# Performance work log

Measured on AMD Instinct MI355X. Metric: run time of the kernel, lower is better.

## Reference

```python
import jax, jax.numpy as jnp
import numpy as np

B = 16      # graphs
NPG = 1024  # nodes per graph (equal-sized, contiguous)
N = B * NPG
K = 12      # knn neighbors
DM = 128    # d_model
DH = 256    # d_hidden = 2*d_model
L = 3       # num_layers
DI = 2 * DM + 4  # msg mlp input dim


def _mlp2(x, W1, b1, W2, b2):
    return jax.nn.silu(x @ W1 + b1) @ W2 + b2


def setup_inputs() -> dict:
    key = jax.random.key(0)
    ks = list(jax.random.split(key, 16))
    def nrm(k, shape, fan):
        return jax.random.normal(k, shape, jnp.float32) / np.float32(np.sqrt(fan))
    return dict(
        x=jax.random.normal(ks[0], (N, 3), jnp.float32),
        batch=(jnp.arange(N) // NPG).astype(jnp.int32),
        in_W1=nrm(ks[1], (3, DM), 3), in_b1=jnp.zeros((DM,), jnp.float32),
        in_W2=nrm(ks[2], (DM, DM), DM), in_b2=jnp.zeros((DM,), jnp.float32),
        msg_W1=nrm(ks[3], (L, DI, DH), DI), msg_b1=jnp.zeros((L, DH), jnp.float32),
        msg_W2=nrm(ks[4], (L, DH, DM), DH), msg_b2=jnp.zeros((L, DM), jnp.float32),
        upd_W1=nrm(ks[5], (L, 2 * DM, DH), 2 * DM), upd_b1=jnp.zeros((L, DH), jnp.float32),
        upd_W2=nrm(ks[6], (L, DH, DM), DH), upd_b2=jnp.zeros((L, DM), jnp.float32),
        norm_w=jnp.ones((L, DM), jnp.float32), norm_b=jnp.zeros((L, DM), jnp.float32),
        norm_ms=jnp.ones((L, DM), jnp.float32),
        gate_W1=nrm(ks[7], (DM, DM), DM), gate_b1=jnp.zeros((DM,), jnp.float32),
        gate_W2=nrm(ks[8], (DM, 1), DM), gate_b2=jnp.zeros((1,), jnp.float32),
        head_W1=nrm(ks[9], (DM, DM), DM), head_b1=jnp.zeros((DM,), jnp.float32),
        head_W2=nrm(ks[10], (DM, 1), DM), head_b2=jnp.zeros((1,), jnp.float32),
    )


def _knn_edges(pos):
    # pos: [N,2]; graphs are contiguous blocks of NPG nodes -> blocked knn
    p3 = pos.reshape(B, NPG, 2)
    d2 = jnp.sum((p3[:, :, None, :] - p3[:, None, :, :]) ** 2, axis=-1)  # [B,n,n]
    d2 = jnp.where(jnp.eye(NPG, dtype=bool)[None], jnp.inf, d2)          # no self loops
    idx = jax.lax.top_k(-d2, K)[1]  # [B,n,K] nearest neighbors (sources)
    offs = (jnp.arange(B) * NPG)[:, None, None]
    src = (idx + offs).reshape(-1)
    dst = jnp.broadcast_to(jnp.arange(N).reshape(B, NPG, 1), (B, NPG, K)).reshape(-1)
    return src, dst


def _graph_norm(h, batch, cnt, w, b, ms):
    # PyG GraphNorm: out = w * (h - ms*mean) / sqrt(var + eps) + b, per-graph stats
    mean = jax.ops.segment_sum(h, batch, B) / cnt
    out = h - mean[batch] * ms
    var = jax.ops.segment_sum(out ** 2, batch, B) / cnt
    return w * out / jnp.sqrt(var + 1e-5)[batch] + b


def _forward(x, batch, in_W1, in_b1, in_W2, in_b2, msg_W1, msg_b1, msg_W2, msg_b2,
             upd_W1, upd_b1, upd_W2, upd_b2, norm_w, norm_b, norm_ms,
             gate_W1, gate_b1, gate_W2, gate_b2, head_W1, head_b1, head_W2, head_b2):
    pos = x[:, 1:3]
    src, dst = _knn_edges(pos)
    # edge_attr = [dx, dy, dist, ds]
    dp = pos[src] - pos[dst]
    dist = jnp.sqrt(jnp.sum(dp ** 2, axis=-1, keepdims=True) + 1e-12)
    ds = x[src, 0:1] - x[dst, 0:1]
    ea = jnp.concatenate([dp, dist, ds], axis=-1)  # [E,4]

    h = _mlp2(x, in_W1, in_b1, in_W2, in_b2)       # [N,DM]
    cnt = jax.ops.segment_sum(jnp.ones((N,), h.dtype), batch, B)[:, None]

    for i in range(L):
        m_in = jnp.concatenate([h[dst], h[src], ea], axis=-1)       # [E,2*DM+4]
        m = _mlp2(m_in, msg_W1[i], msg_b1[i], msg_W2[i], msg_b2[i])  # [E,DM]
        agg = jax.ops.segment_sum(m, dst, N)                         # scatter_add
        dh = _mlp2(jnp.concatenate([h, agg], axis=-1),
                   upd_W1[i], upd_b1[i], upd_W2[i], upd_b2[i])
        h = h + dh  # dropout is identity at inference
        h = _graph_norm(h, batch, cnt, norm_w[i], norm_b[i], norm_ms[i])

    # gated attention pool: segment softmax over gate logits
    gl = (jnp.tanh(h @ gate_W1 + gate_b1) @ gate_W2 + gate_b2)[:, 0]  # [N]
    gmax = jax.ops.segment_max(gl, batch, B)
    e = jnp.exp(gl - gmax[batch])
    a = e / jax.ops.segment_sum(e, batch, B)[batch]
    pooled = jax.ops.segment_sum(h * a[:, None], batch, B)            # [B,DM]

    return _mlp2(pooled, head_W1, head_b1, head_W2, head_b2)[:, 0]    # [B]


def reference(x, batch, in_W1, in_b1, in_W2, in_b2, msg_W1, msg_b1, msg_W2, msg_b2,
              upd_W1, upd_b1, upd_W2, upd_b2, norm_w, norm_b, norm_ms,
              gate_W1, gate_b1, gate_W2, gate_b2, head_W1, head_b1, head_W2, head_b2):
    return _forward(x, batch, in_W1, in_b1, in_W2, in_b2, msg_W1, msg_b1, msg_W2, msg_b2,
                    upd_W1, upd_b1, upd_W2, upd_b2, norm_w, norm_b, norm_ms,
                    gate_W1, gate_b1, gate_W2, gate_b2, head_W1, head_b1, head_W2, head_b2)
```

## Files before the change

kernel.cpp:

```cpp
#include <hip/hip_runtime.h>
#include <math.h>

#define NPTS 16384
#define BGR 16
#define NPGR 1024
#define KNN 12
#define DM 128
#define DH 256
#define NL 3
#define EDG (NPTS*KNN)

typedef unsigned short u16;
typedef unsigned int u32;
typedef __attribute__((ext_vector_type(8))) short short8;
typedef __attribute__((ext_vector_type(4))) float floatx4;

__device__ __forceinline__ float silu_f(float x) {
    return x / (1.0f + __expf(-x));
}
__device__ __forceinline__ u16 f2bf(float f) {
    union { float f; u32 u; } v; v.f = f;
    u32 r = v.u + 0x7fffu + ((v.u >> 16) & 1u);
    return (u16)(r >> 16);
}
__device__ __forceinline__ float bf2f(u16 b) {
    union { u32 u; float f; } v; v.u = ((u32)b) << 16;
    return v.f;
}

#define KPPB 32
__global__ __launch_bounds__(256) void knn_kernel(const float* __restrict__ x,
                                                  int* __restrict__ srcb,
                                                  float* __restrict__ ea) {
#pragma clang fp contract(off)
    __shared__ float px[NPGR], py[NPGR], s0[NPGR];
    __shared__ float sdf[256 * 13];
    __shared__ int   sif[256 * 13];
    __shared__ int   sel[KPPB][KNN];
    int t = threadIdx.x;
    int g   = blockIdx.x / (NPGR / KPPB);
    int blk = blockIdx.x % (NPGR / KPPB);
    int base = g * NPGR;
    for (int j = t; j < NPGR; j += 256) {
        const float* xp = x + (size_t)(base + j) * 3;
        s0[j] = xp[0]; px[j] = xp[1]; py[j] = xp[2];
    }
    __syncthreads();
    int r  = t & 7;
    int pt = t >> 3;
    int il = blk * KPPB + pt;
    float xi = px[il], yi = py[il];
    float nd[KNN]; int ni[KNN];
#pragma unroll
    for (int k = 0; k < KNN; ++k) { nd[k] = 3.4e38f; ni[k] = 0x7fffffff; }
    int j0 = r * 128;
    for (int jj = 0; jj < 128; ++jj) {
        int j = j0 + jj;
        if (j == il) continue;
        float dx = px[j] - xi;
        float dy = py[j] - yi;
        float dx2 = dx * dx;
        float dy2 = dy * dy;
        float d2 = dx2 + dy2;
        if (d2 < nd[KNN-1]) {
            float cd = d2; int ci = j;
#pragma unroll
            for (int k = 0; k < KNN; ++k) {
                bool sw = cd < nd[k];
                float tdv = sw ? nd[k] : cd;
                nd[k] = sw ? cd : nd[k];
                cd = tdv;
                int tiv = sw ? ni[k] : ci;
                ni[k] = sw ? ci : ni[k];
                ci = tiv;
            }
        }
    }
#pragma unroll
    for (int k = 0; k < KNN; ++k) { sdf[t * 13 + k] = nd[k]; sif[t * 13 + k] = ni[k]; }
    __syncthreads();
    if (r == 0) {
        int head[8] = {0,0,0,0,0,0,0,0};
#pragma unroll
        for (int k = 0; k < KNN; ++k) {
            float bd = 3.4e38f; int bi = 0x7fffffff; int bq = 0;
#pragma unroll
            for (int q = 0; q < 8; ++q) {
                int hq = head[q];
                float d = (hq < KNN) ? sdf[(pt * 8 + q) * 13 + hq] : 3.4e38f;
                int  ix = (hq < KNN) ? sif[(pt * 8 + q) * 13 + hq] : 0x7fffffff;
                if (d < bd || (d == bd && ix < bi)) { bd = d; bi = ix; bq = q; }
            }
            head[bq]++;
            sel[pt][k] = bi;
        }
    }
    __syncthreads();
    float x0i = s0[il];
    for (int k = r; k < KNN; k += 8) {
        int j = sel[pt][k];
        size_t e = (size_t)(base + il) * KNN + k;
        srcb[e] = base + j;
        float dpx = px[j] - xi, dpy = py[j] - yi;
        float a = dpx * dpx;
        float b = dpy * dpy;
        float dist = sqrtf(a + b + 1e-12f);
        float dsv = s0[j] - x0i;
        *(float4*)(ea + e * 4) = make_float4(dpx, dpy, dist, dsv);
    }
}

__global__ __launch_bounds__(128) void in_mlp_kernel(const float* __restrict__ x,
    const float* __restrict__ W1, const float* __restrict__ b1,
    const float* __restrict__ W2, const float* __restrict__ b2,
    float* __restrict__ h) {
    __shared__ float hid[8][DM];
    __shared__ float xl[8][3];
    int t = threadIdx.x;
    int nb = blockIdx.x * 8;
    if (t < 24) xl[t / 3][t % 3] = x[(size_t)nb * 3 + t];
    __syncthreads();
    float w0 = W1[t], w1 = W1[DM + t], w2 = W1[2 * DM + t], bb = b1[t];
#pragma unroll
    for (int gi = 0; gi < 8; ++gi) {
        float v = xl[gi][0] * w0 + xl[gi][1] * w1 + xl[gi][2] * w2 + bb;
        hid[gi][t] = silu_f(v);
    }
    __syncthreads();
    float acc[8];
    float b2v = b2[t];
#pragma unroll
    for (int gi = 0; gi < 8; ++gi) acc[gi] = b2v;
    for (int k = 0; k < DM; ++k) {
        float w = W2[k * DM + t];
#pragma unroll
        for (int gi = 0; gi < 8; ++gi) acc[gi] += hid[gi][k] * w;
    }
#pragma unroll
    for (int gi = 0; gi < 8; ++gi) h[(size_t)(nb + gi) * DM + t] = acc[gi];
}

#define MBM 128
#define MBN 128
#define MBK 32
#define MLDA 40

__global__ __launch_bounds__(256) void mgemm_kernel(
    const float* __restrict__ A0, int k0, int lda0,
    const float* __restrict__ A1, int lda1,
    const u16* __restrict__ Wh, const u16* __restrict__ Wl, int K,
    const float* __restrict__ bias,
    const float* __restrict__ resid, int ldres,
    float* __restrict__ out, int ldout,
    int act)
{
    __shared__ __align__(16) u16 Ash[MBM * MLDA];
    __shared__ __align__(16) u16 Asl[MBM * MLDA];
    __shared__ __align__(16) u16 Bsh[MBN * MLDA];
    __shared__ __align__(16) u16 Bsl[MBN * MLDA];
    int t = threadIdx.x;
    int row0 = blockIdx.x * MBM, col0 = blockIdx.y * MBN;
    int lane = t & 63, w = t >> 6;
    int wm = (w >> 1) * 64, wn = (w & 1) * 64;
    int quad = lane >> 4, r15 = lane & 15;
    int srow = t >> 1, scol = (t & 1) * 16;

    floatx4 acc[4][4];
#pragma unroll
    for (int m = 0; m < 4; ++m)
#pragma unroll
        for (int n = 0; n < 4; ++n) acc[m][n] = (floatx4){0.f, 0.f, 0.f, 0.f};

    for (int kt = 0; kt < K; kt += MBK) {
        const float* Ap = (kt < k0)
            ? (A0 + (size_t)(row0 + srow) * lda0 + kt + scol)
            : (A1 + (size_t)(row0 + srow) * lda1 + (kt - k0) + scol);
        float4 a0 = ((const float4*)Ap)[0];
        float4 a1 = ((const float4*)Ap)[1];
        float4 a2 = ((const float4*)Ap)[2];
        float4 a3 = ((const float4*)Ap)[3];
        const u16* Bph = Wh + (size_t)(col0 + srow) * K + kt + scol;
        const u16* Bpl = Wl + (size_t)(col0 + srow) * K + kt + scol;
        uint4 bh0 = ((const uint4*)Bph)[0];
        uint4 bh1 = ((const uint4*)Bph)[1];
        uint4 bl0 = ((const uint4*)Bpl)[0];
        uint4 bl1 = ((const uint4*)Bpl)[1];
        __syncthreads();
        float av[16] = {a0.x,a0.y,a0.z,a0.w, a1.x,a1.y,a1.z,a1.w,
                        a2.x,a2.y,a2.z,a2.w, a3.x,a3.y,a3.z,a3.w};
        u32 uh[8], ul[8];
#pragma unroll
        for (int i = 0; i < 8; ++i) {
            u16 h0 = f2bf(av[2*i]);
            u16 h1 = f2bf(av[2*i+1]);
            u16 l0 = f2bf(av[2*i]   - bf2f(h0));
            u16 l1 = f2bf(av[2*i+1] - bf2f(h1));
            uh[i] = (u32)h0 | ((u32)h1 << 16);
            ul[i] = (u32)l0 | ((u32)l1 << 16);
        }
        uint4* adh = (uint4*)(Ash + srow * MLDA + scol);
        uint4* adl = (uint4*)(Asl + srow * MLDA + scol);
        adh[0] = make_uint4(uh[0],uh[1],uh[2],uh[3]);
        adh[1] = make_uint4(uh[4],uh[5],uh[6],uh[7]);
        adl[0] = make_uint4(ul[0],ul[1],ul[2],ul[3]);
        adl[1] = make_uint4(ul[4],ul[5],ul[6],ul[7]);
        uint4* bdh = (uint4*)(Bsh + srow * MLDA + scol);
        uint4* bdl = (uint4*)(Bsl + srow * MLDA + scol);
        bdh[0] = bh0; bdh[1] = bh1;
        bdl[0] = bl0; bdl[1] = bl1;
        __syncthreads();
        short8 ah[4], alo[4], bhf[4], blf[4];
#pragma unroll
        for (int m = 0; m < 4; ++m) {
            ah[m]  = *(const short8*)(Ash + (wm + m*16 + r15) * MLDA + quad*8);
            alo[m] = *(const short8*)(Asl + (wm + m*16 + r15) * MLDA + quad*8);
        }
#pragma unroll
        for (int n = 0; n < 4; ++n) {
            bhf[n] = *(const short8*)(Bsh + (wn + n*16 + r15) * MLDA + quad*8);
            blf[n] = *(const short8*)(Bsl + (wn + n*16 + r15) * MLDA + quad*8);
        }
#pragma unroll
        for (int m = 0; m < 4; ++m)
#pragma unroll
            for (int n = 0; n < 4; ++n) {
                acc[m][n] = __builtin_amdgcn_mfma_f32_16x16x32_bf16(ah[m],  bhf[n], acc[m][n], 0, 0, 0);
                acc[m][n] = __builtin_amdgcn_mfma_f32_16x16x32_bf16(ah[m],  blf[n], acc[m][n], 0, 0, 0);
                acc[m][n] = __builtin_amdgcn_mfma_f32_16x16x32_bf16(alo[m], bhf[n], acc[m][n], 0, 0, 0);
            }
    }
#pragma unroll
    for (int n = 0; n < 4; ++n) {
        int col = col0 + wn + n*16 + r15;
        float bv = bias ? bias[col] : 0.f;
#pragma unroll
        for (int m = 0; m < 4; ++m) {
#pragma unroll
            for (int reg = 0; reg < 4; ++reg) {
                int row = row0 + wm + m*16 + quad*4 + reg;
                float v = acc[m][n][reg] + bv;
                if (act == 1) v = silu_f(v);
                else if (act == 2) v = tanhf(v);
                if (resid) v += resid[(size_t)row * ldres + col];
                out[(size_t)row * ldout + col] = v;
            }
        }
    }
}

__global__ __launch_bounds__(256) void edge_agg_kernel(
    const float* __restrict__ C, const float* __restrict__ S,
    const int* __restrict__ srcb, const float* __restrict__ ea,
    const float* __restrict__ W1ea,
    float* __restrict__ HS)
{
    int i = blockIdx.x, t = threadIdx.x;
    __shared__ int ss[KNN];
    __shared__ float sea[KNN * 4];
    if (t < KNN) ss[t] = srcb[(size_t)i * KNN + t];
    if (t < KNN * 4) sea[t] = ea[(size_t)i * KNN * 4 + t];
    __syncthreads();
    float base = C[(size_t)i * DH + t];
    float wa = W1ea[t], wb = W1ea[DH + t], wc = W1ea[2 * DH + t], wd = W1ea[3 * DH + t];
    float hs = 0.f;
#pragma unroll
    for (int e = 0; e < KNN; ++e) {
        float v = base + S[(size_t)ss[e] * DH + t]
                + sea[e * 4 + 0] * wa + sea[e * 4 + 1] * wb
                + sea[e * 4 + 2] * wc + sea[e * 4 + 3] * wd;
        hs += silu_f(v);
    }
    HS[(size_t)i * DH + t] = hs;
}

__global__ __launch_bounds__(256) void norm_part_kernel(const float* __restrict__ hn,
                                                        float* __restrict__ psum)
{
    int g = blockIdx.x, blk = blockIdx.y;
    int t = threadIdx.x, d = t & 127, half = t >> 7;
    size_t base = ((size_t)g * NPGR + (size_t)blk * 128 + half * 64) * DM;
    float s = 0.f, s2 = 0.f;
    for (int n = 0; n < 64; ++n) {
        float v = hn[base + (size_t)n * DM + d];
        s += v; s2 += v * v;
    }
    __shared__ float ps[2][DM], ps2[2][DM];
    ps[half][d] = s; ps2[half][d] = s2;
    __syncthreads();
    if (t < DM) {
        psum[(((size_t)g * 8 + blk) * 2 + 0) * DM + d] = ps[0][d] + ps[1][d];
        psum[(((size_t)g * 8 + blk) * 2 + 1) * DM + d] = ps2[0][d] + ps2[1][d];
    }
}

__global__ __launch_bounds__(256) void norm_apply_kernel(const float* __restrict__ hn,
    float* __restrict__ h, const float* __restrict__ psum,
    const float* __restrict__ w, const float* __restrict__ b, const float* __restrict__ ms)
{
    int g = blockIdx.x, blk = blockIdx.y, t = threadIdx.x;
    __shared__ float mmv[DM], rst[DM], wv[DM], bv[DM];
    if (t < DM) {
        float sum = 0.f, sq = 0.f;
        for (int q = 0; q < 8; ++q) {
            sum += psum[(((size_t)g * 8 + q) * 2 + 0) * DM + t];
            sq  += psum[(((size_t)g * 8 + q) * 2 + 1) * DM + t];
        }
        float mean = sum * (1.0f / NPGR);
        float mm = mean * ms[t];
        float var = sq * (1.0f / NPGR) - 2.f * mm * mean + mm * mm;
        mmv[t] = mm;
        rst[t] = 1.0f / sqrtf(var + 1e-5f);
        wv[t] = w[t]; bv[t] = b[t];
    }
    __syncthreads();
    size_t base = ((size_t)g * NPGR + (size_t)blk * 128) * DM;
    for (int i = t; i < 128 * DM; i += 256) {
        int dd = i & 127;
        float v = hn[base + i];
        h[base + i] = wv[dd] * (v - mmv[dd]) * rst[dd] + bv[dd];
    }
}

__global__ __launch_bounds__(256) void gate_dot_kernel(const float* __restrict__ Gh,
    const float* __restrict__ gW2, const float* __restrict__ gb2,
    float* __restrict__ gl)
{
    int t = threadIdx.x, lane = t & 63, w = t >> 6;
    int node = blockIdx.x * 4 + w;
    const float* gp = Gh + (size_t)node * DM;
    float v = gp[lane] * gW2[lane] + gp[lane + 64] * gW2[lane + 64];
    for (int off = 32; off > 0; off >>= 1) v += __shfl_down(v, off, 64);
    if (lane == 0) gl[node] = v + gb2[0];
}

__global__ __launch_bounds__(256) void pool_stats_kernel(const float* __restrict__ gl,
                                                         float* __restrict__ gstat)
{
    int g = blockIdx.x, t = threadIdx.x, lane = t & 63, w = t >> 6;
    __shared__ float red[4];
    const float* gp = gl + (size_t)g * NPGR;
    float mx = -3.4e38f;
    for (int n = t; n < NPGR; n += 256) mx = fmaxf(mx, gp[n]);
    for (int off = 32; off > 0; off >>= 1) mx = fmaxf(mx, __shfl_down(mx, off, 64));
    if (lane == 0) red[w] = mx;
    __syncthreads();
    float gmax = fmaxf(fmaxf(red[0], red[1]), fmaxf(red[2], red[3]));
    __syncthreads();
    float se = 0.f;
    for (int n = t; n < NPGR; n += 256) se += __expf(gp[n] - gmax);
    for (int off = 32; off > 0; off >>= 1) se += __shfl_down(se, off, 64);
    if (lane == 0) red[w] = se;
    __syncthreads();
    if (t == 0) { gstat[g * 2] = gmax; gstat[g * 2 + 1] = red[0] + red[1] + red[2] + red[3]; }
}

__global__ __launch_bounds__(256) void pool_part_kernel(const float* __restrict__ h,
    const float* __restrict__ gl, const float* __restrict__ gstat,
    float* __restrict__ ppool)
{
    int g = blockIdx.x, blk = blockIdx.y;
    int t = threadIdx.x, d = t & 127, half = t >> 7;
    float gmax = gstat[g * 2];
    size_t nbase = (size_t)g * NPGR + (size_t)blk * 128 + half * 64;
    float p = 0.f;
    for (int n = 0; n < 64; ++n)
        p += __expf(gl[nbase + n] - gmax) * h[(nbase + n) * DM + d];
    __shared__ float ps[2][DM];
    ps[half][d] = p;
    __syncthreads();
    if (t < DM) ppool[((size_t)g * 8 + blk) * DM + d] = ps[0][d] + ps[1][d];
}

__global__ __launch_bounds__(128) void pool_head_kernel(const float* __restrict__ ppool,
    const float* __restrict__ gstat,
    const float* __restrict__ hW1, const float* __restrict__ hb1,
    const float* __restrict__ hW2, const float* __restrict__ hb2,
    float* __restrict__ outp)
{
    int g = blockIdx.x, t = threadIdx.x;
    __shared__ float pl[DM];
    __shared__ float red[2];
    float ssum = gstat[g * 2 + 1];
    float p = 0.f;
    for (int q = 0; q < 8; ++q) p += ppool[((size_t)g * 8 + q) * DM + t];
    pl[t] = p / ssum;
    __syncthreads();
    float a = hb1[t];
    for (int k = 0; k < DM; ++k) a += pl[k] * hW1[k * DM + t];
    a = silu_f(a);
    float vv = a * hW2[t];
    int lane = t & 63, w = t >> 6;
    for (int off = 32; off > 0; off >>= 1) vv += __shfl_down(vv, off, 64);
    if (lane == 0) red[w] = vv;
    __syncthreads();
    if (t == 0) outp[g] = red[0] + red[1] + hb2[0];
}

__global__ __launch_bounds__(256) void precompute_kernel(
    const float* __restrict__ msgW2, const float* __restrict__ msgb2,
    const float* __restrict__ updW1, const float* __restrict__ updb1,
    float* __restrict__ W2U, float* __restrict__ bias2)
{
    int bid = blockIdx.x; int t = threadIdx.x;
    if (bid < NL * DH) {
        int l = bid / DH, k = bid % DH;
        const float* w2row = msgW2 + (size_t)l * DH * DM + (size_t)k * DM;
        const float* u1 = updW1 + (size_t)l * 2 * DM * DH;
        float acc = 0.f;
        for (int j = 0; j < DM; ++j) acc += w2row[j] * u1[(size_t)(DM + j) * DH + t];
        W2U[(size_t)l * DH * DH + (size_t)k * DH + t] = acc;
    } else {
        int l = bid - NL * DH;
        const float* u1 = updW1 + (size_t)l * 2 * DM * DH;
        const float* b2 = msgb2 + (size_t)l * DM;
        float acc = updb1[(size_t)l * DH + t];
        for (int j = 0; j < DM; ++j) acc += 12.0f * b2[j] * u1[(size_t)(DM + j) * DH + t];
        bias2[(size_t)l * DH + t] = acc;
    }
}

struct WJob { const float* src; u16* dh; u16* dl; int K, N, ldd, off; };
struct WJobs { WJob j[16]; };
__global__ __launch_bounds__(256) void wprep_kernel(WJobs jobs) {
    WJob jb = jobs.j[blockIdx.y];
    int n = blockIdx.x;
    if (n >= jb.N) return;
    for (int k = threadIdx.x; k < jb.K; k += 256) {
        float v = jb.src[(size_t)k * jb.N + n];
        u16 hi = f2bf(v);
        u16 lo = f2bf(v - bf2f(hi));
        jb.dh[(size_t)n * jb.ldd + jb.off + k] = hi;
        jb.dl[(size_t)n * jb.ldd + jb.off + k] = lo;
    }
}

extern "C" void kernel_launch(void* const* d_in, const int* in_sizes, int n_in,
                              void* d_out, int out_size, void* d_ws, size_t ws_size,
                              hipStream_t stream) {
    const float* x     = (const float*)d_in[0];
    const float* inW1  = (const float*)d_in[2];
    const float* inb1  = (const float*)d_in[3];
    const float* inW2  = (const float*)d_in[4];
    const float* inb2  = (const float*)d_in[5];
    const float* msgW1 = (const float*)d_in[6];
    const float* msgb1 = (const float*)d_in[7];
    const float* msgW2 = (const float*)d_in[8];
    const float* msgb2 = (const float*)d_in[9];
    const float* updW1 = (const float*)d_in[10];
    const float* updb1 = (const float*)d_in[11];
    const float* updW2 = (const float*)d_in[12];
    const float* updb2 = (const float*)d_in[13];
    const float* nw    = (const float*)d_in[14];
    const float* nb    = (const float*)d_in[15];
    const float* nms   = (const float*)d_in[16];
    const float* gW1   = (const float*)d_in[17];
    const float* gb1   = (const float*)d_in[18];
    const float* gW2   = (const float*)d_in[19];
    const float* gb2   = (const float*)d_in[20];
    const float* hW1   = (const float*)d_in[21];
    const float* hb1   = (const float*)d_in[22];
    const float* hW2   = (const float*)d_in[23];
    const float* hb2   = (const float*)d_in[24];
    float* outp = (float*)d_out;

    float* ws    = (float*)d_ws;
    float* h     = ws;
    float* Cb    = h + (size_t)NPTS * DM;
    float* Sb    = Cb + (size_t)NPTS * DH;
    float* HSb   = Sb + (size_t)NPTS * DH;
    float* W2U   = HSb + (size_t)NPTS * DH;
    float* bias2 = W2U + (size_t)NL * DH * DH;
    float* glb   = bias2 + NL * DH;
    int*   srcb  = (int*)(glb + NPTS);
    float* eab   = (float*)(srcb + EDG);
    float* psum  = eab + (size_t)EDG * 4;
    float* gstat = psum + 16 * 8 * 2 * DM;
    float* ppool = gstat + 32;
    u16* wsp = (u16*)(ppool + 16 * 8 * DM);
    u16* WCh = wsp;                 u16* WCl = WCh + (size_t)NL * DH * DM;
    u16* WSh = WCl + (size_t)NL * DH * DM;  u16* WSl = WSh + (size_t)NL * DH * DM;
    u16* WTh = WSl + (size_t)NL * DH * DM;  u16* WTl = WTh + (size_t)NL * DH * 384;
    u16* WUh = WTl + (size_t)NL * DH * 384; u16* WUl = WUh + (size_t)NL * DM * DH;
    u16* WGh = WUl + (size_t)NL * DM * DH;  u16* WGl = WGh + (size_t)DM * DM;

    hipLaunchKernelGGL(precompute_kernel, dim3(NL * DH + NL), dim3(DH), 0, stream,
                       msgW2, msgb2, updW1, updb1, W2U, bias2);

    WJobs jobs;
    int ji = 0;
    for (int l = 0; l < NL; ++l) {
        jobs.j[ji++] = WJob{ msgW1 + (size_t)l * 260 * DH,             WCh + (size_t)l * DH * DM, WCl + (size_t)l * DH * DM, 128, 256, 128, 0 };
        jobs.j[ji++] = WJob{ msgW1 + (size_t)l * 260 * DH + 128 * DH,  WSh + (size_t)l * DH * DM, WSl + (size_t)l * DH * DM, 128, 256, 128, 0 };
        jobs.j[ji++] = WJob{ updW1 + (size_t)l * 256 * DH,             WTh + (size_t)l * DH * 384, WTl + (size_t)l * DH * 384, 128, 256, 384, 0 };
        jobs.j[ji++] = WJob{ W2U   + (size_t)l * DH * DH,              WTh + (size_t)l * DH * 384, WTl + (size_t)l * DH * 384, 256, 256, 384, 128 };
        jobs.j[ji++] = WJob{ updW2 + (size_t)l * DH * DM,              WUh + (size_t)l * DM * DH, WUl + (size_t)l * DM * DH, 256, 128, 256, 0 };
    }
    jobs.j[ji++] = WJob{ gW1, WGh, WGl, 128, 128, 128, 0 };
    hipLaunchKernelGGL(wprep_kernel, dim3(256, 16), dim3(256), 0, stream, jobs);

    hipLaunchKernelGGL(knn_kernel, dim3(NPTS / KPPB), dim3(256), 0, stream, x, srcb, eab);
    hipLaunchKernelGGL(in_mlp_kernel, dim3(NPTS / 8), dim3(128), 0, stream,
                       x, inW1, inb1, inW2, inb2, h);

    for (int l = 0; l < NL; ++l) {
        const float* W1l = msgW1 + (size_t)l * 260 * DH;
        hipLaunchKernelGGL(mgemm_kernel, dim3(NPTS / MBM, DH / MBN), dim3(256), 0, stream,
            h, DM, DM, (const float*)nullptr, 0,
            WCh + (size_t)l * DH * DM, WCl + (size_t)l * DH * DM, DM,
            msgb1 + (size_t)l * DH, (const float*)nullptr, 0, Cb, DH, 0);
        hipLaunchKernelGGL(mgemm_kernel, dim3(NPTS / MBM, DH / MBN), dim3(256), 0, stream,
            h, DM, DM, (const float*)nullptr, 0,
            WSh + (size_t)l * DH * DM, WSl + (size_t)l * DH * DM, DM,
            (const float*)nullptr, (const float*)nullptr, 0, Sb, DH, 0);
        hipLaunchKernelGGL(edge_agg_kernel, dim3(NPTS), dim3(DH), 0, stream,
            Cb, Sb, srcb, eab, W1l + (size_t)2 * DM * DH, HSb);
        hipLaunchKernelGGL(mgemm_kernel, dim3(NPTS / MBM, DH / MBN), dim3(256), 0, stream,
            h, DM, DM, HSb, DH,
            WTh + (size_t)l * DH * 384, WTl + (size_t)l * DH * 384, 384,
            bias2 + (size_t)l * DH, (const float*)nullptr, 0, Cb, DH, 1);
        hipLaunchKernelGGL(mgemm_kernel, dim3(NPTS / MBM, DM / MBN), dim3(256), 0, stream,
            Cb, DH, DH, (const float*)nullptr, 0,
            WUh + (size_t)l * DM * DH, WUl + (size_t)l * DM * DH, DH,
            updb2 + (size_t)l * DM, h, DM, Sb, DM, 0);
        hipLaunchKernelGGL(norm_part_kernel, dim3(BGR, 8), dim3(256), 0, stream, Sb, psum);
        hipLaunchKernelGGL(norm_apply_kernel, dim3(BGR, 8), dim3(256), 0, stream,
            Sb, h, psum, nw + (size_t)l * DM, nb + (size_t)l * DM, nms + (size_t)l * DM);
    }

    hipLaunchKernelGGL(mgemm_kernel, dim3(NPTS / MBM, DM / MBN), dim3(256), 0, stream,
        h, DM, DM, (const float*)nullptr, 0,
        WGh, WGl, DM, gb1, (const float*)nullptr, 0, Cb, DM, 2);
    hipLaunchKernelGGL(gate_dot_kernel, dim3(NPTS / 4), dim3(256), 0, stream,
        Cb, gW2, gb2, glb);

    hipLaunchKernelGGL(pool_stats_kernel, dim3(BGR), dim3(256), 0, stream, glb, gstat);
    hipLaunchKernelGGL(pool_part_kernel, dim3(BGR, 8), dim3(256), 0, stream, h, glb, gstat, ppool);
    hipLaunchKernelGGL(pool_head_kernel, dim3(BGR), dim3(128), 0, stream,
        ppool, gstat, hW1, hb1, hW2, hb2, outp);
}
```

Baseline: 627.1 us.

## Merge C/S projection GEMMs, halve GEMM M-tile, and split KNN scan wider

Fuses the two per-layer projection GEMMs on h into one GEMM with a concatenated 512-column weight and interleaved CS output, with bias applied only to the first 256 columns. The mgemm M-tile is halved to 64 rows to double the block count for better CU occupancy. The KNN kernel now handles 16 points per block with 16 scanning threads each, which shortens each thread's serial insertion loop but doubles the merge width. Buffers are reshuffled so the update output goes to HSb. The CS layout also gives strided reads in edge_agg.

```diff
diff --git a/kernel.cpp b/kernel.cpp
--- a/kernel.cpp
+++ b/kernel.cpp
@@ -28,14 +28,15 @@
     return v.f;
 }
 
-#define KPPB 32
+#define KPPB 16
+#define PSTR 209
 __global__ __launch_bounds__(256) void knn_kernel(const float* __restrict__ x,
                                                   int* __restrict__ srcb,
                                                   float* __restrict__ ea) {
 #pragma clang fp contract(off)
     __shared__ float px[NPGR], py[NPGR], s0[NPGR];
-    __shared__ float sdf[256 * 13];
-    __shared__ int   sif[256 * 13];
+    __shared__ float sdf[KPPB * PSTR];
+    __shared__ int   sif[KPPB * PSTR];
     __shared__ int   sel[KPPB][KNN];
     int t = threadIdx.x;
     int g   = blockIdx.x / (NPGR / KPPB);
@@ -46,15 +47,15 @@
         s0[j] = xp[0]; px[j] = xp[1]; py[j] = xp[2];
     }
     __syncthreads();
-    int r  = t & 7;
-    int pt = t >> 3;
+    int r  = t & 15;
+    int pt = t >> 4;
     int il = blk * KPPB + pt;
     float xi = px[il], yi = py[il];
     float nd[KNN]; int ni[KNN];
 #pragma unroll
     for (int k = 0; k < KNN; ++k) { nd[k] = 3.4e38f; ni[k] = 0x7fffffff; }
-    int j0 = r * 128;
-    for (int jj = 0; jj < 128; ++jj) {
+    int j0 = r * 64;
+    for (int jj = 0; jj < 64; ++jj) {
         int j = j0 + jj;
         if (j == il) continue;
         float dx = px[j] - xi;
@@ -77,18 +78,23 @@
         }
     }
 #pragma unroll
-    for (int k = 0; k < KNN; ++k) { sdf[t * 13 + k] = nd[k]; sif[t * 13 + k] = ni[k]; }
+    for (int k = 0; k < KNN; ++k) {
+        sdf[pt * PSTR + r * 13 + k] = nd[k];
+        sif[pt * PSTR + r * 13 + k] = ni[k];
+    }
     __syncthreads();
     if (r == 0) {
-        int head[8] = {0,0,0,0,0,0,0,0};
+        int head[16];
+#pragma unroll
+        for (int q = 0; q < 16; ++q) head[q] = 0;
 #pragma unroll
         for (int k = 0; k < KNN; ++k) {
             float bd = 3.4e38f; int bi = 0x7fffffff; int bq = 0;
 #pragma unroll
-            for (int q = 0; q < 8; ++q) {
+            for (int q = 0; q < 16; ++q) {
                 int hq = head[q];
-                float d = (hq < KNN) ? sdf[(pt * 8 + q) * 13 + hq] : 3.4e38f;
-                int  ix = (hq < KNN) ? sif[(pt * 8 + q) * 13 + hq] : 0x7fffffff;
+                float d = (hq < KNN) ? sdf[pt * PSTR + q * 13 + hq] : 3.4e38f;
+                int  ix = (hq < KNN) ? sif[pt * PSTR + q * 13 + hq] : 0x7fffffff;
                 if (d < bd || (d == bd && ix < bi)) { bd = d; bi = ix; bq = q; }
             }
             head[bq]++;
@@ -96,11 +102,12 @@
         }
     }
     __syncthreads();
-    float x0i = s0[il];
-    for (int k = r; k < KNN; k += 8) {
+    if (r < KNN) {
+        int k = r;
         int j = sel[pt][k];
         size_t e = (size_t)(base + il) * KNN + k;
         srcb[e] = base + j;
+        float x0i = s0[il];
         float dpx = px[j] - xi, dpy = py[j] - yi;
         float a = dpx * dpx;
         float b = dpy * dpy;
@@ -140,7 +147,7 @@
     for (int gi = 0; gi < 8; ++gi) h[(size_t)(nb + gi) * DM + t] = acc[gi];
 }
 
-#define MBM 128
+#define MBM 64
 #define MBN 128
 #define MBK 32
 #define MLDA 40
@@ -149,7 +156,7 @@
     const float* __restrict__ A0, int k0, int lda0,
     const float* __restrict__ A1, int lda1,
     const u16* __restrict__ Wh, const u16* __restrict__ Wl, int K,
-    const float* __restrict__ bias,
+    const float* __restrict__ bias, int biasN,
     const float* __restrict__ resid, int ldres,
     float* __restrict__ out, int ldout,
     int act)
@@ -161,36 +168,34 @@
     int t = threadIdx.x;
     int row0 = blockIdx.x * MBM, col0 = blockIdx.y * MBN;
     int lane = t & 63, w = t >> 6;
-    int wm = (w >> 1) * 64, wn = (w & 1) * 64;
+    int wm = (w >> 1) * 32, wn = (w & 1) * 64;
     int quad = lane >> 4, r15 = lane & 15;
-    int srow = t >> 1, scol = (t & 1) * 16;
-
-    floatx4 acc[4][4];
-#pragma unroll
-    for (int m = 0; m < 4; ++m)
+    int arow = t >> 2, acol = (t & 3) * 8;
+    int brow = t >> 1, bcol = (t & 1) * 16;
+
+    floatx4 acc[2][4];
+#pragma unroll
+    for (int m = 0; m < 2; ++m)
 #pragma unroll
         for (int n = 0; n < 4; ++n) acc[m][n] = (floatx4){0.f, 0.f, 0.f, 0.f};
 
     for (int kt = 0; kt < K; kt += MBK) {
         const float* Ap = (kt < k0)
-            ? (A0 + (size_t)(row0 + srow) * lda0 + kt + scol)
-            : (A1 + (size_t)(row0 + srow) * lda1 + (kt - k0) + scol);
+            ? (A0 + (size_t)(row0 + arow) * lda0 + kt + acol)
+            : (A1 + (size_t)(row0 + arow) * lda1 + (kt - k0) + acol);
         float4 a0 = ((const float4*)Ap)[0];
         float4 a1 = ((const float4*)Ap)[1];
-        float4 a2 = ((const float4*)Ap)[2];
-        float4 a3 = ((const float4*)Ap)[3];
-        const u16* Bph = Wh + (size_t)(col0 + srow) * K + kt + scol;
-        const u16* Bpl = Wl + (size_t)(col0 + srow) * K + kt + scol;
+        const u16* Bph = Wh + (size_t)(col0 + brow) * K + kt + bcol;
+        const u16* Bpl = Wl + (size_t)(col0 + brow) * K + kt + bcol;
         uint4 bh0 = ((const uint4*)Bph)[0];
         uint4 bh1 = ((const uint4*)Bph)[1];
         uint4 bl0 = ((const uint4*)Bpl)[0];
         uint4 bl1 = ((const uint4*)Bpl)[1];
         __syncthreads();
-        float av[16] = {a0.x,a0.y,a0.z,a0.w, a1.x,a1.y,a1.z,a1.w,
-                        a2.x,a2.y,a2.z,a2.w, a3.x,a3.y,a3.z,a3.w};
-        u32 uh[8], ul[8];
-#pragma unroll
-        for (int i = 0; i < 8; ++i) {
+        float av[8] = {a0.x,a0.y,a0.z,a0.w, a1.x,a1.y,a1.z,a1.w};
+        u32 uh[4], ul[4];
+#pragma unroll
+        for (int i = 0; i < 4; ++i) {
             u16 h0 = f2bf(av[2*i]);
             u16 h1 = f2bf(av[2*i+1]);
             u16 l0 = f2bf(av[2*i]   - bf2f(h0));
@@ -198,20 +203,16 @@
             uh[i] = (u32)h0 | ((u32)h1 << 16);
             ul[i] = (u32)l0 | ((u32)l1 << 16);
         }
-        uint4* adh = (uint4*)(Ash + srow * MLDA + scol);
-        uint4* adl = (uint4*)(Asl + srow * MLDA + scol);
-        adh[0] = make_uint4(uh[0],uh[1],uh[2],uh[3]);
-        adh[1] = make_uint4(uh[4],uh[5],uh[6],uh[7]);
-        adl[0] = make_uint4(ul[0],ul[1],ul[2],ul[3]);
-        adl[1] = make_uint4(ul[4],ul[5],ul[6],ul[7]);
-        uint4* bdh = (uint4*)(Bsh + srow * MLDA + scol);
-        uint4* bdl = (uint4*)(Bsl + srow * MLDA + scol);
+        *(uint4*)(Ash + arow * MLDA + acol) = make_uint4(uh[0],uh[1],uh[2],uh[3]);
+        *(uint4*)(Asl + arow * MLDA + acol) = make_uint4(ul[0],ul[1],ul[2],ul[3]);
+        uint4* bdh = (uint4*)(Bsh + brow * MLDA + bcol);
+        uint4* bdl = (uint4*)(Bsl + brow * MLDA + bcol);
         bdh[0] = bh0; bdh[1] = bh1;
         bdl[0] = bl0; bdl[1] = bl1;
         __syncthreads();
-        short8 ah[4], alo[4], bhf[4], blf[4];
-#pragma unroll
-        for (int m = 0; m < 4; ++m) {
+        short8 ah[2], alo[2], bhf[4], blf[4];
+#pragma unroll
+        for (int m = 0; m < 2; ++m) {
             ah[m]  = *(const short8*)(Ash + (wm + m*16 + r15) * MLDA + quad*8);
             alo[m] = *(const short8*)(Asl + (wm + m*16 + r15) * MLDA + quad*8);
         }
@@ -221,7 +222,7 @@
             blf[n] = *(const short8*)(Bsl + (wn + n*16 + r15) * MLDA + quad*8);
         }
 #pragma unroll
-        for (int m = 0; m < 4; ++m)
+        for (int m = 0; m < 2; ++m)
 #pragma unroll
             for (int n = 0; n < 4; ++n) {
                 acc[m][n] = __builtin_amdgcn_mfma_f32_16x16x32_bf16(ah[m],  bhf[n], acc[m][n], 0, 0, 0);
@@ -232,9 +233,9 @@
 #pragma unroll
     for (int n = 0; n < 4; ++n) {
         int col = col0 + wn + n*16 + r15;
-        float bv = bias ? bias[col] : 0.f;
-#pragma unroll
-        for (int m = 0; m < 4; ++m) {
+        float bv = (bias && col < biasN) ? bias[col] : 0.f;
+#pragma unroll
+        for (int m = 0; m < 2; ++m) {
 #pragma unroll
             for (int reg = 0; reg < 4; ++reg) {
                 int row = row0 + wm + m*16 + quad*4 + reg;
@@ -249,7 +250,7 @@
 }
 
 __global__ __launch_bounds__(256) void edge_agg_kernel(
-    const float* __restrict__ C, const float* __restrict__ S,
+    const float* __restrict__ CS,
     const int* __restrict__ srcb, const float* __restrict__ ea,
     const float* __restrict__ W1ea,
     float* __restrict__ HS)
@@ -260,12 +261,12 @@
     if (t < KNN) ss[t] = srcb[(size_t)i * KNN + t];
     if (t < KNN * 4) sea[t] = ea[(size_t)i * KNN * 4 + t];
     __syncthreads();
-    float base = C[(size_t)i * DH + t];
+    float base = CS[(size_t)i * 512 + t];
     float wa = W1ea[t], wb = W1ea[DH + t], wc = W1ea[2 * DH + t], wd = W1ea[3 * DH + t];
     float hs = 0.f;
 #pragma unroll
     for (int e = 0; e < KNN; ++e) {
-        float v = base + S[(size_t)ss[e] * DH + t]
+        float v = base + CS[(size_t)ss[e] * 512 + 256 + t]
                 + sea[e * 4 + 0] * wa + sea[e * 4 + 1] * wb
                 + sea[e * 4 + 2] * wc + sea[e * 4 + 3] * wd;
         hs += silu_f(v);
@@ -465,9 +466,8 @@
 
     float* ws    = (float*)d_ws;
     float* h     = ws;
-    float* Cb    = h + (size_t)NPTS * DM;
-    float* Sb    = Cb + (size_t)NPTS * DH;
-    float* HSb   = Sb + (size_t)NPTS * DH;
+    float* CSb   = h + (size_t)NPTS * DM;
+    float* HSb   = CSb + (size_t)NPTS * 512;
     float* W2U   = HSb + (size_t)NPTS * DH;
     float* bias2 = W2U + (size_t)NL * DH * DH;
     float* glb   = bias2 + NL * DH;
@@ -477,11 +477,10 @@
     float* gstat = psum + 16 * 8 * 2 * DM;
     float* ppool = gstat + 32;
     u16* wsp = (u16*)(ppool + 16 * 8 * DM);
-    u16* WCh = wsp;                 u16* WCl = WCh + (size_t)NL * DH * DM;
-    u16* WSh = WCl + (size_t)NL * DH * DM;  u16* WSl = WSh + (size_t)NL * DH * DM;
-    u16* WTh = WSl + (size_t)NL * DH * DM;  u16* WTl = WTh + (size_t)NL * DH * 384;
-    u16* WUh = WTl + (size_t)NL * DH * 384; u16* WUl = WUh + (size_t)NL * DM * DH;
-    u16* WGh = WUl + (size_t)NL * DM * DH;  u16* WGl = WGh + (size_t)DM * DM;
+    u16* WCSh = wsp;                                 u16* WCSl = WCSh + (size_t)NL * 512 * DM;
+    u16* WTh = WCSl + (size_t)NL * 512 * DM;         u16* WTl = WTh + (size_t)NL * DH * 384;
+    u16* WUh = WTl + (size_t)NL * DH * 384;          u16* WUl = WUh + (size_t)NL * DM * DH;
+    u16* WGh = WUl + (size_t)NL * DM * DH;           u16* WGl = WGh + (size_t)DM * DM;
 
     hipLaunchKernelGGL(precompute_kernel, dim3(NL * DH + NL), dim3(DH), 0, stream,
                        msgW2, msgb2, updW1, updb1, W2U, bias2);
@@ -489,11 +488,11 @@
     WJobs jobs;
     int ji = 0;
     for (int l = 0; l < NL; ++l) {
-        jobs.j[ji++] = WJob{ msgW1 + (size_t)l * 260 * DH,             WCh + (size_t)l * DH * DM, WCl + (size_t)l * DH * DM, 128, 256, 128, 0 };
-        jobs.j[ji++] = WJob{ msgW1 + (size_t)l * 260 * DH + 128 * DH,  WSh + (size_t)l * DH * DM, WSl + (size_t)l * DH * DM, 128, 256, 128, 0 };
-        jobs.j[ji++] = WJob{ updW1 + (size_t)l * 256 * DH,             WTh + (size_t)l * DH * 384, WTl + (size_t)l * DH * 384, 128, 256, 384, 0 };
-        jobs.j[ji++] = WJob{ W2U   + (size_t)l * DH * DH,              WTh + (size_t)l * DH * 384, WTl + (size_t)l * DH * 384, 256, 256, 384, 128 };
-        jobs.j[ji++] = WJob{ updW2 + (size_t)l * DH * DM,              WUh + (size_t)l * DM * DH, WUl + (size_t)l * DM * DH, 256, 128, 256, 0 };
+        jobs.j[ji++] = WJob{ msgW1 + (size_t)l * 260 * DH,            WCSh + (size_t)l * 512 * DM,            WCSl + (size_t)l * 512 * DM,            128, 256, 128, 0 };
+        jobs.j[ji++] = WJob{ msgW1 + (size_t)l * 260 * DH + 128 * DH, WCSh + (size_t)l * 512 * DM + 256 * DM, WCSl + (size_t)l * 512 * DM + 256 * DM, 128, 256, 128, 0 };
+        jobs.j[ji++] = WJob{ updW1 + (size_t)l * 256 * DH,            WTh + (size_t)l * DH * 384, WTl + (size_t)l * DH * 384, 128, 256, 384, 0 };
+        jobs.j[ji++] = WJob{ W2U   + (size_t)l * DH * DH,             WTh + (size_t)l * DH * 384, WTl + (size_t)l * DH * 384, 256, 256, 384, 128 };
+        jobs.j[ji++] = WJob{ updW2 + (size_t)l * DH * DM,             WUh + (size_t)l * DM * DH, WUl + (size_t)l * DM * DH, 256, 128, 256, 0 };
     }
     jobs.j[ji++] = WJob{ gW1, WGh, WGl, 128, 128, 128, 0 };
     hipLaunchKernelGGL(wprep_kernel, dim3(256, 16), dim3(256), 0, stream, jobs);
@@ -504,34 +503,30 @@
 
     for (int l = 0; l < NL; ++l) {
         const float* W1l = msgW1 + (size_t)l * 260 * DH;
-        hipLaunchKernelGGL(mgemm_kernel, dim3(NPTS / MBM, DH / MBN), dim3(256), 0, stream,
+        hipLaunchKernelGGL(mgemm_kernel, dim3(NPTS / MBM, 512 / MBN), dim3(256), 0, stream,
             h, DM, DM, (const float*)nullptr, 0,
-            WCh + (size_t)l * DH * DM, WCl + (size_t)l * DH * DM, DM,
-            msgb1 + (size_t)l * DH, (const float*)nullptr, 0, Cb, DH, 0);
-        hipLaunchKernelGGL(mgemm_kernel, dim3(NPTS / MBM, DH / MBN), dim3(256), 0, stream,
-            h, DM, DM, (const float*)nullptr, 0,
-            WSh + (size_t)l * DH * DM, WSl + (size_t)l * DH * DM, DM,
-            (const float*)nullptr, (const float*)nullptr, 0, Sb, DH, 0);
+            WCSh + (size_t)l * 512 * DM, WCSl + (size_t)l * 512 * DM, DM,
+            msgb1 + (size_t)l * DH, 256, (const float*)nullptr, 0, CSb, 512, 0);
         hipLaunchKernelGGL(edge_agg_kernel, dim3(NPTS), dim3(DH), 0, stream,
-            Cb, Sb, srcb, eab, W1l + (size_t)2 * DM * DH, HSb);
+            CSb, srcb, eab, W1l + (size_t)2 * DM * DH, HSb);
         hipLaunchKernelGGL(mgemm_kernel, dim3(NPTS / MBM, DH / MBN), dim3(256), 0, stream,
             h, DM, DM, HSb, DH,
             WTh + (size_t)l * DH * 384, WTl + (size_t)l * DH * 384, 384,
-            bias2 + (size_t)l * DH, (const float*)nullptr, 0, Cb, DH, 1);
+            bias2 + (size_t)l * DH, DH, (const float*)nullptr, 0, CSb, 512, 1);
         hipLaunchKernelGGL(mgemm_kernel, dim3(NPTS / MBM, DM / MBN), dim3(256), 0, stream,
-            Cb, DH, DH, (const float*)nullptr, 0,
+            CSb, 512, 512, (const float*)nullptr, 0,
             WUh + (size_t)l * DM * DH, WUl + (size_t)l * DM * DH, DH,
-            updb2 + (size_t)l * DM, h, DM, Sb, DM, 0);
-        hipLaunchKernelGGL(norm_part_kernel, dim3(BGR, 8), dim3(256), 0, stream, Sb, psum);
+            updb2 + (size_t)l * DM, DM, h, DM, HSb, DM, 0);
+        hipLaunchKernelGGL(norm_part_kernel, dim3(BGR, 8), dim3(256), 0, stream, HSb, psum);
         hipLaunchKernelGGL(norm_apply_kernel, dim3(BGR, 8), dim3(256), 0, stream,
-            Sb, h, psum, nw + (size_t)l * DM, nb + (size_t)l * DM, nms + (size_t)l * DM);
+            HSb, h, psum, nw + (size_t)l * DM, nb + (size_t)l * DM, nms + (size_t)l * DM);
     }
 
     hipLaunchKernelGGL(mgemm_kernel, dim3(NPTS / MBM, DM / MBN), dim3(256), 0, stream,
         h, DM, DM, (const float*)nullptr, 0,
-        WGh, WGl, DM, gb1, (const float*)nullptr, 0, Cb, DM, 2);
+        WGh, WGl, DM, gb1, DM, (const float*)nullptr, 0, CSb, DM, 2);
     hipLaunchKernelGGL(gate_dot_kernel, dim3(NPTS / 4), dim3(256), 0, stream,
-        Cb, gW2, gb2, glb);
+        CSb, gW2, gb2, glb);
 
     hipLaunchKernelGGL(pool_stats_kernel, dim3(BGR), dim3(256), 0, stream, glb, gstat);
     hipLaunchKernelGGL(pool_part_kernel, dim3(BGR, 8), dim3(256), 0, stream, h, glb, gstat, ppool);
```

Result: faster. 541.7 us (-13.6%).
